# Kernel optimization log

Measured on AMD Instinct MI355X. Metric: run time of the kernel, lower is better.

The kernel has to match this reference:

```python
import jax, jax.numpy as jnp
import numpy as np

# Dimensions (see shape_source)
N, M, C = 64, 300, 768          # batch, tokens (=max_frames), token dim
LAMB, G, K = 2, 8, 64           # expansion, groups, clusters
GS = LAMB * C // G              # group_size = 192
DESC = K * GS                   # 12288 NeXtVLAD descriptor dim
NB, NCLS = 512, 701             # bottleneck, classes


def setup_inputs() -> dict:
    key = jax.random.key(0)
    ks = jax.random.split(key, 8)
    w = lambda i, shape: jax.random.normal(ks[i], shape, jnp.float32) * 0.02
    return {
        "features": jax.random.normal(ks[0], (N, M + 1, C), jnp.float32),
        # NeXtVLAD_block params
        "fc0_w": w(1, (LAMB * C, C)), "fc0_b": jnp.zeros((LAMB * C,), jnp.float32),
        "fcgk_w": w(2, (G * K, LAMB * C)), "fcgk_b": jnp.zeros((G * K,), jnp.float32),
        "fcg_w": w(3, (G, LAMB * C)), "fcg_b": jnp.zeros((G,), jnp.float32),
        "bn0_g": jnp.ones((M,), jnp.float32), "bn0_b": jnp.zeros((M,), jnp.float32),
        "cw2": jax.random.uniform(ks[4], (1, GS, K), jnp.float32),
        "bn1_g": jnp.ones((1,), jnp.float32), "bn1_b": jnp.zeros((1,), jnp.float32),
        # ClassBlock params (Linear -> BN -> Linear classifier)
        "cls_fc_w": w(5, (NB, DESC)), "cls_fc_b": jnp.zeros((NB,), jnp.float32),
        "cls_bn_g": jnp.ones((NB,), jnp.float32), "cls_bn_b": jnp.zeros((NB,), jnp.float32),
        "cls_w": w(6, (NCLS, NB)), "cls_b": jnp.zeros((NCLS,), jnp.float32),
    }


def reference(features, fc0_w, fc0_b, fcgk_w, fcgk_b, fcg_w, fcg_b,
              bn0_g, bn0_b, cw2, bn1_g, bn1_b,
              cls_fc_w, cls_fc_b, cls_bn_g, cls_bn_b, cls_w, cls_b):
    # Drop CLS token -> local descriptors (N, M, C). (transpose+vector2image
    # in the torch code is a pure rearrangement back to (N, M, C) tokens.)
    x = features[:, 1:]
    # 1) expand D -> lamb*D
    x_dot = jnp.einsum('nmc,ec->nme', x, fc0_w) + fc0_b           # (N, M, lamb*C)
    # 2) group: (N, M*G, group_size)
    x_tilde = x_dot.reshape(-1, M * G, GS)
    # 3) soft assignment logits, BN over the frame axis (inference-mode BN:
    #    running stats 0/1 -> pure per-frame affine), softmax over clusters
    WgkX = jnp.einsum('nme,fe->nmf', x_dot, fcgk_w) + fcgk_b      # (N, M, G*K)
    WgkX = WgkX * bn0_g[None, :, None] + bn0_b[None, :, None]
    alpha_gk = jax.nn.softmax(WgkX.reshape(-1, M * G, K), axis=-1)
    # 4) sigmoid group attention
    alpha_g = jax.nn.sigmoid(jnp.einsum('nme,ge->nmg', x_dot, fcg_w) + fcg_b)
    alpha_g = alpha_g.reshape(-1, M * G, 1)
    activation = alpha_gk * alpha_g                                # (N, M*G, K)
    # 5) aggregate residuals: vlad = act^T x_tilde - a_sum * centers
    a = jnp.sum(activation, axis=1, keepdims=True) * cw2           # (N, GS, K)
    vlad = jnp.einsum('npk,npd->ndk', activation, x_tilde) - a     # (N, GS, K)
    # 6) L1-normalize over group_size dim (F.normalize(vlad, 1): p=1, dim=1)
    norm = jnp.maximum(jnp.sum(jnp.abs(vlad), axis=1, keepdims=True), 1e-12)
    vlad = (vlad / norm).reshape(-1, DESC)
    # bn1 = BatchNorm1d(1), inference mode -> scalar affine
    vlad = vlad * bn1_g[0] + bn1_b[0]
    # ClassBlock: Linear -> BN (inference affine) -> classifier Linear
    f = jnp.einsum('nd,bd->nb', vlad, cls_fc_w) + cls_fc_b         # (N, NB)
    f = f * cls_bn_g + cls_bn_b
    cls = jnp.einsum('nb,cb->nc', f, cls_w) + cls_b                # (N, NCLS)
    return (cls, f)
```

## Files before the change

### kernel.cpp

```cpp
#include <hip/hip_runtime.h>
#include <hip/hip_bf16.h>

#define NN 64
#define MM 300
#define CC 768
#define EE 1536
#define GG 8
#define KK 64
#define FF 512
#define GS 192
#define PP 2400
#define DESC 12288
#define NMROWS 19200
#define NB 512
#define NCLS 701

typedef _Float16 v8h __attribute__((ext_vector_type(8)));
typedef _Float16 v4h __attribute__((ext_vector_type(4)));
typedef float    v4f __attribute__((ext_vector_type(4)));

#define GLOAD_LDS16(g, s) \
    __builtin_amdgcn_global_load_lds( \
        (const __attribute__((address_space(1))) void*)(g), \
        (__attribute__((address_space(3))) void*)(s), 16, 0, 0)

__global__ __launch_bounds__(256)
void pack_x_k(const float* __restrict__ f, _Float16* __restrict__ o)
{
    int idx = blockIdx.x * 256 + threadIdx.x;
    int row = idx / 192;
    int c4  = (idx - row * 192) * 4;
    int n = row / 300, m = row - n * 300;
    float4 v = *(const float4*)(f + ((size_t)(n * 301 + m + 1)) * CC + c4);
    v4h h = { (_Float16)v.x, (_Float16)v.y, (_Float16)v.z, (_Float16)v.w };
    *(v4h*)(o + (size_t)row * CC + c4) = h;
}

__global__ __launch_bounds__(256)
void pack_w_k(const float* __restrict__ s, _Float16* __restrict__ o, int n4)
{
    int idx = blockIdx.x * 256 + threadIdx.x;
    if (idx >= n4) return;
    float4 v = *(const float4*)(s + (size_t)idx * 4);
    v4h h = { (_Float16)v.x, (_Float16)v.y, (_Float16)v.z, (_Float16)v.w };
    *(v4h*)(o + (size_t)idx * 4) = h;
}

template<bool OUTF16, bool BN0, bool SOFTGATE>
__global__ __launch_bounds__(256)
void hgemm_nt(const _Float16* __restrict__ A, const _Float16* __restrict__ B,
              const float* __restrict__ bias,
              const float* __restrict__ bn_g, const float* __restrict__ bn_b,
              const float* __restrict__ sig,
              void* __restrict__ Cout, int Ndim, int Kdim)
{
    __shared__ _Float16 As[128 * 32];
    __shared__ _Float16 Bs[128 * 32];

    const int tid  = threadIdx.x;
    const int wave = tid >> 6, lane = tid & 63;
    const int wr   = wave >> 1, wc = wave & 1;
    const int row0 = blockIdx.y * 128, col0 = blockIdx.x * 128;

    const int l0 = tid, l1 = 256 + tid;
    const _Float16* ga0 = A + (size_t)(row0 + (l0 >> 2)) * Kdim + (l0 & 3) * 8;
    const _Float16* ga1 = A + (size_t)(row0 + (l1 >> 2)) * Kdim + (l1 & 3) * 8;
    const _Float16* gb0 = B + (size_t)(col0 + (l0 >> 2)) * Kdim + (l0 & 3) * 8;
    const _Float16* gb1 = B + (size_t)(col0 + (l1 >> 2)) * Kdim + (l1 & 3) * 8;
    _Float16* sa0 = As + wave * 512;
    _Float16* sa1 = As + 2048 + wave * 512;
    _Float16* sb0 = Bs + wave * 512;
    _Float16* sb1 = Bs + 2048 + wave * 512;

    v4f acc[4][4];
    #pragma unroll
    for (int i = 0; i < 4; ++i)
        #pragma unroll
        for (int j = 0; j < 4; ++j)
            acc[i][j] = (v4f){0.f, 0.f, 0.f, 0.f};

    const int fm = lane & 15, fq = lane >> 4;
    const _Float16* arp = As + (wr * 64 + fm) * 32 + fq * 8;
    const _Float16* brp = Bs + (wc * 64 + fm) * 32 + fq * 8;

    for (int kt = 0; kt < Kdim; kt += 32) {
        GLOAD_LDS16(ga0 + kt, sa0);
        GLOAD_LDS16(ga1 + kt, sa1);
        GLOAD_LDS16(gb0 + kt, sb0);
        GLOAD_LDS16(gb1 + kt, sb1);
        __syncthreads();

        v8h af[4], bf[4];
        #pragma unroll
        for (int i = 0; i < 4; ++i) af[i] = *(const v8h*)(arp + i * 16 * 32);
        #pragma unroll
        for (int j = 0; j < 4; ++j) bf[j] = *(const v8h*)(brp + j * 16 * 32);
        #pragma unroll
        for (int i = 0; i < 4; ++i)
            #pragma unroll
            for (int j = 0; j < 4; ++j)
                acc[i][j] = __builtin_amdgcn_mfma_f32_16x16x32_f16(
                    af[i], bf[j], acc[i][j], 0, 0, 0);
        __syncthreads();
    }

    float bj[4];
    #pragma unroll
    for (int j = 0; j < 4; ++j) bj[j] = bias[col0 + wc * 64 + j * 16 + fm];

    if (SOFTGATE) {
        const int gidx = (col0 >> 6) + wc;
        #pragma unroll
        for (int i = 0; i < 4; ++i) {
            #pragma unroll
            for (int r = 0; r < 4; ++r) {
                int grow = row0 + wr * 64 + i * 16 + fq * 4 + r;
                int n = grow / 300, mm = grow - n * 300;
                float g = bn_g[mm], bb = bn_b[mm];
                float v[4];
                #pragma unroll
                for (int j = 0; j < 4; ++j)
                    v[j] = (acc[i][j][r] + bj[j]) * g + bb;
                float mx = fmaxf(fmaxf(v[0], v[1]), fmaxf(v[2], v[3]));
                #pragma unroll
                for (int w = 1; w < 16; w <<= 1) mx = fmaxf(mx, __shfl_xor(mx, w));
                float e[4], s = 0.f;
                #pragma unroll
                for (int j = 0; j < 4; ++j) { e[j] = __expf(v[j] - mx); s += e[j]; }
                #pragma unroll
                for (int w = 1; w < 16; w <<= 1) s += __shfl_xor(s, w);
                float gate = sig[(size_t)grow * GG + gidx];
                float inv = gate / s;
                float* cp = (float*)Cout + (size_t)grow * Ndim + col0 + wc * 64;
                #pragma unroll
                for (int j = 0; j < 4; ++j) cp[j * 16 + fm] = e[j] * inv;
            }
        }
        return;
    }

    #pragma unroll
    for (int i = 0; i < 4; ++i) {
        #pragma unroll
        for (int r = 0; r < 4; ++r) {
            int grow = row0 + wr * 64 + i * 16 + fq * 4 + r;
            float g = 1.f, bb = 0.f;
            if (BN0) { int m = grow % 300; g = bn_g[m]; bb = bn_b[m]; }
            #pragma unroll
            for (int j = 0; j < 4; ++j) {
                int gcol = col0 + wc * 64 + j * 16 + fm;
                float v = acc[i][j][r] + bj[j];
                if (BN0) v = v * g + bb;
                if (OUTF16)
                    ((_Float16*)Cout)[(size_t)grow * Ndim + gcol] = (_Float16)v;
                else
                    ((float*)Cout)[(size_t)grow * Ndim + gcol] = v;
            }
        }
    }
}

__global__ __launch_bounds__(256)
void alpha_sig_k(const _Float16* __restrict__ xdot, const float* __restrict__ fcg_w,
                 const float* __restrict__ fcg_b, float* __restrict__ sig)
{
    __shared__ float W[GG * EE];
    for (int i = threadIdx.x; i < GG * EE; i += 256) W[i] = fcg_w[i];
    __syncthreads();

    const int wave = threadIdx.x >> 6;
    const int lane = threadIdx.x & 63;

    for (int rr = 0; rr < 4; ++rr) {
        int row = blockIdx.x * 16 + wave * 4 + rr;
        const _Float16* xr = xdot + (size_t)row * EE;
        float acc[GG] = {};
        for (int c = lane; c < EE; c += 64) {
            float xv = (float)xr[c];
            #pragma unroll
            for (int g = 0; g < GG; ++g) acc[g] = fmaf(xv, W[g * EE + c], acc[g]);
        }
        float myval = 0.f;
        #pragma unroll
        for (int g = 0; g < GG; ++g) {
            float s = acc[g];
            #pragma unroll
            for (int o = 32; o; o >>= 1) s += __shfl_xor(s, o);
            if (lane == g) myval = s + fcg_b[g];
        }
        if (lane < GG) {
            sig[(size_t)row * GG + lane] = 1.f / (1.f + __expf(-myval));
        }
    }
}

__global__ __launch_bounds__(256)
void asum_k(const float* __restrict__ act, float* __restrict__ a)
{
    int n = blockIdx.x;
    int k = threadIdx.x & 63, q = threadIdx.x >> 6;
    const float* base = act + (size_t)n * PP * 64;
    float s = 0.f;
    for (int p = q * 600; p < (q + 1) * 600; ++p) s += base[(size_t)p * 64 + k];
    __shared__ float part[4][64];
    part[q][k] = s;
    __syncthreads();
    if (threadIdx.x < 64)
        a[n * 64 + threadIdx.x] = part[0][threadIdx.x] + part[1][threadIdx.x]
                                + part[2][threadIdx.x] + part[3][threadIdx.x];
}

__global__ __launch_bounds__(256)
void vlad_ps_k(const float* __restrict__ act, const _Float16* __restrict__ xdot,
               float* __restrict__ part)
{
    const int dt = blockIdx.x, n = blockIdx.y, ps = blockIdx.z;
    const int d0 = dt * 64;
    const int p0 = ps * 300, pend = p0 + 300;
    __shared__ float As[16][64];
    __shared__ float Xs[16][64];
    const int tid = threadIdx.x;
    const int tx = tid & 15, ty = tid >> 4;
    const int kb = tx * 4, db = ty * 4;
    const float* actn = act + (size_t)n * PP * 64;
    const _Float16* xn = xdot + (size_t)n * MM * EE;
    float acc[4][4] = {};

    const int lpp = tid >> 4, lk4 = (tid & 15) << 2;
    for (int pc = p0; pc < pend; pc += 16) {
        int p = pc + lpp;
        float4 av = make_float4(0.f, 0.f, 0.f, 0.f);
        float x0 = 0.f, x1 = 0.f, x2 = 0.f, x3 = 0.f;
        if (p < pend) {
            av = *(const float4*)(actn + (size_t)p * 64 + lk4);
            v4h xv = *(const v4h*)(xn + (size_t)(p >> 3) * EE + (p & 7) * GS + d0 + lk4);
            x0 = (float)xv[0]; x1 = (float)xv[1]; x2 = (float)xv[2]; x3 = (float)xv[3];
        }
        *(float4*)&As[lpp][lk4] = av;
        Xs[lpp][lk4 + 0] = x0; Xs[lpp][lk4 + 1] = x1;
        Xs[lpp][lk4 + 2] = x2; Xs[lpp][lk4 + 3] = x3;
        __syncthreads();
        #pragma unroll
        for (int q = 0; q < 16; ++q) {
            float4 a4 = *(const float4*)&As[q][kb];
            float4 x4 = *(const float4*)&Xs[q][db];
            float aa[4] = {a4.x, a4.y, a4.z, a4.w};
            float xx[4] = {x4.x, x4.y, x4.z, x4.w};
            #pragma unroll
            for (int i = 0; i < 4; ++i)
                #pragma unroll
                for (int j = 0; j < 4; ++j)
                    acc[i][j] = fmaf(xx[i], aa[j], acc[i][j]);
        }
        __syncthreads();
    }

    float* pp = part + ((size_t)ps * NN + n) * DESC;
    #pragma unroll
    for (int i = 0; i < 4; ++i) {
        int dd = d0 + db + i;
        float4 o = {acc[i][0], acc[i][1], acc[i][2], acc[i][3]};
        *(float4*)(pp + (size_t)dd * 64 + kb) = o;
    }
}

__global__ __launch_bounds__(256)
void vlad_reduce_k(const float* __restrict__ part, const float* __restrict__ a,
                   const float* __restrict__ cw2, float* __restrict__ vlad)
{
    int idx = blockIdx.x * 256 + threadIdx.x;
    float s = 0.f;
    #pragma unroll
    for (int ps = 0; ps < 8; ++ps) s += part[(size_t)ps * (NN * DESC) + idx];
    int k = idx & 63;
    int d = (idx >> 6) % GS;
    int n = idx / DESC;
    vlad[idx] = s - a[n * 64 + k] * cw2[d * 64 + k];
}

__global__ __launch_bounds__(256)
void norm_k(float* __restrict__ vlad, const float* __restrict__ bn1g,
            const float* __restrict__ bn1b)
{
    int n = blockIdx.x;
    float* v = vlad + (size_t)n * DESC;
    int k = threadIdx.x & 63, q = threadIdx.x >> 6;
    float s = 0.f;
    for (int d = q * 48; d < q * 48 + 48; ++d) s += fabsf(v[d * 64 + k]);
    __shared__ float part[4][64];
    __shared__ float inv[64];
    part[q][k] = s;
    __syncthreads();
    if (threadIdx.x < 64) {
        float t = part[0][threadIdx.x] + part[1][threadIdx.x]
                + part[2][threadIdx.x] + part[3][threadIdx.x];
        inv[threadIdx.x] = 1.f / fmaxf(t, 1e-12f);
    }
    __syncthreads();
    float g = bn1g[0], b = bn1b[0];
    for (int idx = threadIdx.x; idx < DESC; idx += 256) {
        v[idx] = v[idx] * inv[idx & 63] * g + b;
    }
}

__global__ __launch_bounds__(256)
void fsplit_k(const float* __restrict__ vlad, const float* __restrict__ W,
              float* __restrict__ part)
{
    const int bcol0 = (blockIdx.x & 7) * 64;
    const int ks = blockIdx.x >> 3;
    const int kc0 = ks * 256;
    __shared__ float Vs[32][68];
    __shared__ float Ws[32][68];
    const int tid = threadIdx.x, tx = tid & 15, ty = tid >> 4;
    float acc[4][4] = {};

    for (int kc = kc0; kc < kc0 + 256; kc += 32) {
        #pragma unroll
        for (int it = 0; it < 2; ++it) {
            int sl = tid + it * 256;
            int rr = sl >> 3, k4 = (sl & 7) << 2;
            float4 v = *(const float4*)(vlad + (size_t)rr * DESC + kc + k4);
            Vs[k4+0][rr] = v.x; Vs[k4+1][rr] = v.y; Vs[k4+2][rr] = v.z; Vs[k4+3][rr] = v.w;
            float4 w = *(const float4*)(W + (size_t)(bcol0 + rr) * DESC + kc + k4);
            Ws[k4+0][rr] = w.x; Ws[k4+1][rr] = w.y; Ws[k4+2][rr] = w.z; Ws[k4+3][rr] = w.w;
        }
        __syncthreads();
        #pragma unroll
        for (int q = 0; q < 32; ++q) {
            float4 wv = *(const float4*)&Ws[q][tx*4];
            float4 vv = *(const float4*)&Vs[q][ty*4];
            float wa[4] = {wv.x, wv.y, wv.z, wv.w};
            float va[4] = {vv.x, vv.y, vv.z, vv.w};
            #pragma unroll
            for (int i = 0; i < 4; ++i)
                #pragma unroll
                for (int j = 0; j < 4; ++j)
                    acc[i][j] = fmaf(va[i], wa[j], acc[i][j]);
        }
        __syncthreads();
    }
    float* p = part + (size_t)ks * (NN * NB);
    #pragma unroll
    for (int i = 0; i < 4; ++i) {
        int n = ty * 4 + i;
        float4 o = {acc[i][0], acc[i][1], acc[i][2], acc[i][3]};
        *(float4*)(p + (size_t)n * NB + bcol0 + tx*4) = o;
    }
}

__global__ __launch_bounds__(256)
void freduce_k(const float* __restrict__ part, const float* __restrict__ bias,
               const float* __restrict__ bng, const float* __restrict__ bnb,
               float* __restrict__ f)
{
    int idx = blockIdx.x * 256 + threadIdx.x;
    float s = 0.f;
    for (int ks = 0; ks < 48; ++ks) s += part[(size_t)ks * (NN * NB) + idx];
    int b = idx & (NB - 1);
    f[idx] = (s + bias[b]) * bng[b] + bnb[b];
}

__global__ __launch_bounds__(256)
void cls_k(const float* __restrict__ f, const float* __restrict__ W,
           const float* __restrict__ bias, float* __restrict__ out)
{
    const int c0 = blockIdx.x * 64;
    __shared__ float Fs[32][68];
    __shared__ float Ws[32][68];
    const int tid = threadIdx.x, tx = tid & 15, ty = tid >> 4;
    float acc[4][4] = {};

    for (int kc = 0; kc < NB; kc += 32) {
        #pragma unroll
        for (int it = 0; it < 2; ++it) {
            int sl = tid + it * 256;
            int rr = sl >> 3, k4 = (sl & 7) << 2;
            float4 v = *(const float4*)(f + (size_t)rr * NB + kc + k4);
            Fs[k4+0][rr] = v.x; Fs[k4+1][rr] = v.y; Fs[k4+2][rr] = v.z; Fs[k4+3][rr] = v.w;
            int c = c0 + rr;
            float4 w = (c < NCLS) ? *(const float4*)(W + (size_t)c * NB + kc + k4)
                                  : make_float4(0.f, 0.f, 0.f, 0.f);
            Ws[k4+0][rr] = w.x; Ws[k4+1][rr] = w.y; Ws[k4+2][rr] = w.z; Ws[k4+3][rr] = w.w;
        }
        __syncthreads();
        #pragma unroll
        for (int q = 0; q < 32; ++q) {
            float4 wv = *(const float4*)&Ws[q][tx*4];
            float4 fv = *(const float4*)&Fs[q][ty*4];
            float wa[4] = {wv.x, wv.y, wv.z, wv.w};
            float fa[4] = {fv.x, fv.y, fv.z, fv.w};
            #pragma unroll
            for (int i = 0; i < 4; ++i)
                #pragma unroll
                for (int j = 0; j < 4; ++j)
                    acc[i][j] = fmaf(fa[i], wa[j], acc[i][j]);
        }
        __syncthreads();
    }
    #pragma unroll
    for (int i = 0; i < 4; ++i) {
        int n = ty * 4 + i;
        #pragma unroll
        for (int j = 0; j < 4; ++j) {
            int c = c0 + tx * 4 + j;
            if (c < NCLS) out[(size_t)n * NCLS + c] = acc[i][j] + bias[c];
        }
    }
}

extern "C" void kernel_launch(void* const* d_in, const int* in_sizes, int n_in,
                              void* d_out, int out_size, void* d_ws, size_t ws_size,
                              hipStream_t stream)
{
    const float* features = (const float*)d_in[0];
    const float* fc0_w    = (const float*)d_in[1];
    const float* fc0_b    = (const float*)d_in[2];
    const float* fcgk_w   = (const float*)d_in[3];
    const float* fcgk_b   = (const float*)d_in[4];
    const float* fcg_w    = (const float*)d_in[5];
    const float* fcg_b    = (const float*)d_in[6];
    const float* bn0_g    = (const float*)d_in[7];
    const float* bn0_b    = (const float*)d_in[8];
    const float* cw2      = (const float*)d_in[9];
    const float* bn1_g    = (const float*)d_in[10];
    const float* bn1_b    = (const float*)d_in[11];
    const float* cls_fc_w = (const float*)d_in[12];
    const float* cls_fc_b = (const float*)d_in[13];
    const float* cls_bn_g = (const float*)d_in[14];
    const float* cls_bn_b = (const float*)d_in[15];
    const float* cls_w    = (const float*)d_in[16];
    const float* cls_b    = (const float*)d_in[17];

    char* ws = (char*)d_ws;
    _Float16* xf16   = (_Float16*)(ws + 0);
    _Float16* w1f16  = (_Float16*)(ws + 29491200);
    _Float16* w2f16  = (_Float16*)(ws + 31850496);
    _Float16* xdot16 = (_Float16*)(ws + 33423360);
    float*    act    = (float*)   (ws + 92405760);
    float*    sigma  = (float*)   (ws + 131727360);
    float*    asum   = (float*)   (ws + 132341760);
    float*    vlad   = (float*)   (ws + 132358144);
    float*    vpart  = (float*)   (ws + 135503872);
    float*    fpart  = (float*)   (ws + 160669696);

    float* cls_out = (float*)d_out;
    float* f_out   = cls_out + NN * NCLS;

    dim3 blk(256);

    pack_x_k<<<14400, blk, 0, stream>>>(features, xf16);
    pack_w_k<<<1152, blk, 0, stream>>>(fc0_w, w1f16, EE * CC / 4);
    pack_w_k<<<768, blk, 0, stream>>>(fcgk_w, w2f16, FF * EE / 4);

    hgemm_nt<true, false, false><<<dim3(12, 150), blk, 0, stream>>>(
        xf16, w1f16, fc0_b, nullptr, nullptr, nullptr, xdot16, EE, CC);

    alpha_sig_k<<<1200, blk, 0, stream>>>(xdot16, fcg_w, fcg_b, sigma);

    hgemm_nt<false, true, true><<<dim3(4, 150), blk, 0, stream>>>(
        xdot16, w2f16, fcgk_b, bn0_g, bn0_b, sigma, act, FF, EE);

    asum_k<<<64, blk, 0, stream>>>(act, asum);

    vlad_ps_k<<<dim3(3, 64, 8), blk, 0, stream>>>(act, xdot16, vpart);
    vlad_reduce_k<<<3072, blk, 0, stream>>>(vpart, asum, cw2, vlad);

    norm_k<<<64, blk, 0, stream>>>(vlad, bn1_g, bn1_b);

    fsplit_k<<<384, blk, 0, stream>>>(vlad, cls_fc_w, fpart);
    freduce_k<<<128, blk, 0, stream>>>(fpart, cls_fc_b, cls_bn_g, cls_bn_b, f_out);

    cls_k<<<11, blk, 0, stream>>>(f_out, cls_w, cls_b, cls_out);
}
```

Measured before the change: 519.8 us.

## Fold fc0 into assignment and gate weights, swizzle LDS, store activations in fp16

```diff
diff --git a/kernel.cpp b/kernel.cpp
--- a/kernel.cpp
+++ b/kernel.cpp
@@ -46,7 +46,70 @@
     *(v4h*)(o + (size_t)idx * 4) = h;
 }
 
-template<bool OUTF16, bool BN0, bool SOFTGATE>
+__global__ __launch_bounds__(256)
+void transpose_w1_k(const float* __restrict__ w1, _Float16* __restrict__ o)
+{
+    __shared__ float T[64][65];
+    const int c0 = blockIdx.x * 64, e0 = blockIdx.y * 64;
+    const int tc = threadIdx.x & 63, te = threadIdx.x >> 6;
+    #pragma unroll
+    for (int r = 0; r < 16; ++r) {
+        int el = te * 16 + r;
+        T[el][tc] = w1[(size_t)(e0 + el) * CC + c0 + tc];
+    }
+    __syncthreads();
+    #pragma unroll
+    for (int r = 0; r < 16; ++r) {
+        int cl = te * 16 + r;
+        o[(size_t)(c0 + cl) * EE + e0 + tc] = (_Float16)T[tc][cl];
+    }
+}
+
+__global__ __launch_bounds__(256)
+void biasc_k(const float* __restrict__ w2, const float* __restrict__ b2,
+             const float* __restrict__ wg, const float* __restrict__ bg,
+             const float* __restrict__ b0, float* __restrict__ biasc)
+{
+    int f = blockIdx.x;
+    const float* row = (f < FF) ? (w2 + (size_t)f * EE) : (wg + (size_t)(f - FF) * EE);
+    float s = 0.f;
+    for (int e = threadIdx.x; e < EE; e += 256) s += row[e] * b0[e];
+    __shared__ float red[256];
+    red[threadIdx.x] = s;
+    __syncthreads();
+    for (int o = 128; o; o >>= 1) {
+        if (threadIdx.x < o) red[threadIdx.x] += red[threadIdx.x + o];
+        __syncthreads();
+    }
+    if (threadIdx.x == 0)
+        biasc[f] = red[0] + ((f < FF) ? b2[f] : bg[f - FF]);
+}
+
+__global__ __launch_bounds__(256)
+void wgc_k(const float* __restrict__ wg, const float* __restrict__ w1,
+           float* __restrict__ wgc)
+{
+    const int c = blockIdx.x * 64 + (threadIdx.x & 63);
+    const int q = threadIdx.x >> 6;
+    float acc[GG] = {};
+    for (int e = q * 384; e < q * 384 + 384; ++e) {
+        float w1v = w1[(size_t)e * CC + c];
+        #pragma unroll
+        for (int g = 0; g < GG; ++g) acc[g] = fmaf(wg[g * EE + e], w1v, acc[g]);
+    }
+    __shared__ float red[4][GG][64];
+    #pragma unroll
+    for (int g = 0; g < GG; ++g) red[q][g][threadIdx.x & 63] = acc[g];
+    __syncthreads();
+    if (threadIdx.x < 64) {
+        #pragma unroll
+        for (int g = 0; g < GG; ++g)
+            wgc[g * CC + c] = red[0][g][threadIdx.x] + red[1][g][threadIdx.x]
+                            + red[2][g][threadIdx.x] + red[3][g][threadIdx.x];
+    }
+}
+
+template<bool OUTF16, bool BN0, bool SOFTGATE, bool BIAS>
 __global__ __launch_bounds__(256)
 void hgemm_nt(const _Float16* __restrict__ A, const _Float16* __restrict__ B,
               const float* __restrict__ bias,
@@ -62,11 +125,12 @@
     const int wr   = wave >> 1, wc = wave & 1;
     const int row0 = blockIdx.y * 128, col0 = blockIdx.x * 128;
 
-    const int l0 = tid, l1 = 256 + tid;
-    const _Float16* ga0 = A + (size_t)(row0 + (l0 >> 2)) * Kdim + (l0 & 3) * 8;
-    const _Float16* ga1 = A + (size_t)(row0 + (l1 >> 2)) * Kdim + (l1 & 3) * 8;
-    const _Float16* gb0 = B + (size_t)(col0 + (l0 >> 2)) * Kdim + (l0 & 3) * 8;
-    const _Float16* gb1 = B + (size_t)(col0 + (l1 >> 2)) * Kdim + (l1 & 3) * 8;
+    const int r0 = tid >> 2, cs = tid & 3;
+    const int cc = cs ^ ((r0 >> 1) & 3);
+    const _Float16* ga0 = A + (size_t)(row0 + r0) * Kdim + cc * 8;
+    const _Float16* ga1 = A + (size_t)(row0 + r0 + 64) * Kdim + cc * 8;
+    const _Float16* gb0 = B + (size_t)(col0 + r0) * Kdim + cc * 8;
+    const _Float16* gb1 = B + (size_t)(col0 + r0 + 64) * Kdim + cc * 8;
     _Float16* sa0 = As + wave * 512;
     _Float16* sa1 = As + 2048 + wave * 512;
     _Float16* sb0 = Bs + wave * 512;
@@ -80,8 +144,9 @@
             acc[i][j] = (v4f){0.f, 0.f, 0.f, 0.f};
 
     const int fm = lane & 15, fq = lane >> 4;
-    const _Float16* arp = As + (wr * 64 + fm) * 32 + fq * 8;
-    const _Float16* brp = Bs + (wc * 64 + fm) * 32 + fq * 8;
+    const int sw = (fm >> 1) & 3;
+    const _Float16* arp = As + (wr * 64 + fm) * 32 + (fq ^ sw) * 8;
+    const _Float16* brp = Bs + (wc * 64 + fm) * 32 + (fq ^ sw) * 8;
 
     for (int kt = 0; kt < Kdim; kt += 32) {
         GLOAD_LDS16(ga0 + kt, sa0);
@@ -106,7 +171,8 @@
 
     float bj[4];
     #pragma unroll
-    for (int j = 0; j < 4; ++j) bj[j] = bias[col0 + wc * 64 + j * 16 + fm];
+    for (int j = 0; j < 4; ++j)
+        bj[j] = BIAS ? bias[col0 + wc * 64 + j * 16 + fm] : 0.f;
 
     if (SOFTGATE) {
         const int gidx = (col0 >> 6) + wc;
@@ -131,9 +197,15 @@
                 for (int w = 1; w < 16; w <<= 1) s += __shfl_xor(s, w);
                 float gate = sig[(size_t)grow * GG + gidx];
                 float inv = gate / s;
-                float* cp = (float*)Cout + (size_t)grow * Ndim + col0 + wc * 64;
-                #pragma unroll
-                for (int j = 0; j < 4; ++j) cp[j * 16 + fm] = e[j] * inv;
+                if (OUTF16) {
+                    _Float16* cp = (_Float16*)Cout + (size_t)grow * Ndim + col0 + wc * 64;
+                    #pragma unroll
+                    for (int j = 0; j < 4; ++j) cp[j * 16 + fm] = (_Float16)(e[j] * inv);
+                } else {
+                    float* cp = (float*)Cout + (size_t)grow * Ndim + col0 + wc * 64;
+                    #pragma unroll
+                    for (int j = 0; j < 4; ++j) cp[j * 16 + fm] = e[j] * inv;
+                }
             }
         }
         return;
@@ -161,11 +233,11 @@
 }
 
 __global__ __launch_bounds__(256)
-void alpha_sig_k(const _Float16* __restrict__ xdot, const float* __restrict__ fcg_w,
-                 const float* __restrict__ fcg_b, float* __restrict__ sig)
-{
-    __shared__ float W[GG * EE];
-    for (int i = threadIdx.x; i < GG * EE; i += 256) W[i] = fcg_w[i];
+void alpha_sig_k(const _Float16* __restrict__ x, const float* __restrict__ wgc,
+                 const float* __restrict__ bgc, float* __restrict__ sig)
+{
+    __shared__ float W[GG * CC];
+    for (int i = threadIdx.x; i < GG * CC; i += 256) W[i] = wgc[i];
     __syncthreads();
 
     const int wave = threadIdx.x >> 6;
@@ -173,12 +245,12 @@
 
     for (int rr = 0; rr < 4; ++rr) {
         int row = blockIdx.x * 16 + wave * 4 + rr;
-        const _Float16* xr = xdot + (size_t)row * EE;
+        const _Float16* xr = x + (size_t)row * CC;
         float acc[GG] = {};
-        for (int c = lane; c < EE; c += 64) {
+        for (int c = lane; c < CC; c += 64) {
             float xv = (float)xr[c];
             #pragma unroll
-            for (int g = 0; g < GG; ++g) acc[g] = fmaf(xv, W[g * EE + c], acc[g]);
+            for (int g = 0; g < GG; ++g) acc[g] = fmaf(xv, W[g * CC + c], acc[g]);
         }
         float myval = 0.f;
         #pragma unroll
@@ -186,7 +258,7 @@
             float s = acc[g];
             #pragma unroll
             for (int o = 32; o; o >>= 1) s += __shfl_xor(s, o);
-            if (lane == g) myval = s + fcg_b[g];
+            if (lane == g) myval = s + bgc[g];
         }
         if (lane < GG) {
             sig[(size_t)row * GG + lane] = 1.f / (1.f + __expf(-myval));
@@ -195,23 +267,24 @@
 }
 
 __global__ __launch_bounds__(256)
-void asum_k(const float* __restrict__ act, float* __restrict__ a)
-{
-    int n = blockIdx.x;
-    int k = threadIdx.x & 63, q = threadIdx.x >> 6;
-    const float* base = act + (size_t)n * PP * 64;
+void asum_ps_k(const _Float16* __restrict__ act, float* __restrict__ apart)
+{
+    const int ps = blockIdx.x, n = blockIdx.y;
+    const int k = threadIdx.x & 63, q = threadIdx.x >> 6;
+    const _Float16* base = act + ((size_t)n * PP + ps * 300 + q * 75) * 64 + k;
     float s = 0.f;
-    for (int p = q * 600; p < (q + 1) * 600; ++p) s += base[(size_t)p * 64 + k];
+    for (int p = 0; p < 75; ++p) s += (float)base[(size_t)p * 64];
     __shared__ float part[4][64];
     part[q][k] = s;
     __syncthreads();
     if (threadIdx.x < 64)
-        a[n * 64 + threadIdx.x] = part[0][threadIdx.x] + part[1][threadIdx.x]
-                                + part[2][threadIdx.x] + part[3][threadIdx.x];
-}
-
-__global__ __launch_bounds__(256)
-void vlad_ps_k(const float* __restrict__ act, const _Float16* __restrict__ xdot,
+        apart[((size_t)ps * NN + n) * 64 + threadIdx.x] =
+            part[0][threadIdx.x] + part[1][threadIdx.x]
+          + part[2][threadIdx.x] + part[3][threadIdx.x];
+}
+
+__global__ __launch_bounds__(256)
+void vlad_ps_k(const _Float16* __restrict__ act, const _Float16* __restrict__ xdot,
                float* __restrict__ part)
 {
     const int dt = blockIdx.x, n = blockIdx.y, ps = blockIdx.z;
@@ -222,21 +295,23 @@
     const int tid = threadIdx.x;
     const int tx = tid & 15, ty = tid >> 4;
     const int kb = tx * 4, db = ty * 4;
-    const float* actn = act + (size_t)n * PP * 64;
-    const _Float16* xn = xdot + (size_t)n * MM * EE;
+    const _Float16* actn = act + (size_t)n * PP * 64;
+    const _Float16* xn   = xdot + (size_t)n * MM * EE;
     float acc[4][4] = {};
 
     const int lpp = tid >> 4, lk4 = (tid & 15) << 2;
     for (int pc = p0; pc < pend; pc += 16) {
         int p = pc + lpp;
-        float4 av = make_float4(0.f, 0.f, 0.f, 0.f);
+        float a0 = 0.f, a1 = 0.f, a2 = 0.f, a3 = 0.f;
         float x0 = 0.f, x1 = 0.f, x2 = 0.f, x3 = 0.f;
         if (p < pend) {
-            av = *(const float4*)(actn + (size_t)p * 64 + lk4);
+            v4h avh = *(const v4h*)(actn + (size_t)p * 64 + lk4);
+            a0 = (float)avh[0]; a1 = (float)avh[1]; a2 = (float)avh[2]; a3 = (float)avh[3];
             v4h xv = *(const v4h*)(xn + (size_t)(p >> 3) * EE + (p & 7) * GS + d0 + lk4);
             x0 = (float)xv[0]; x1 = (float)xv[1]; x2 = (float)xv[2]; x3 = (float)xv[3];
         }
-        *(float4*)&As[lpp][lk4] = av;
+        As[lpp][lk4 + 0] = a0; As[lpp][lk4 + 1] = a1;
+        As[lpp][lk4 + 2] = a2; As[lpp][lk4 + 3] = a3;
         Xs[lpp][lk4 + 0] = x0; Xs[lpp][lk4 + 1] = x1;
         Xs[lpp][lk4 + 2] = x2; Xs[lpp][lk4 + 3] = x3;
         __syncthreads();
@@ -265,7 +340,7 @@
 }
 
 __global__ __launch_bounds__(256)
-void vlad_reduce_k(const float* __restrict__ part, const float* __restrict__ a,
+void vlad_reduce_k(const float* __restrict__ part, const float* __restrict__ apart,
                    const float* __restrict__ cw2, float* __restrict__ vlad)
 {
     int idx = blockIdx.x * 256 + threadIdx.x;
@@ -275,7 +350,10 @@
     int k = idx & 63;
     int d = (idx >> 6) % GS;
     int n = idx / DESC;
-    vlad[idx] = s - a[n * 64 + k] * cw2[d * 64 + k];
+    float a = 0.f;
+    #pragma unroll
+    for (int ps = 0; ps < 8; ++ps) a += apart[((size_t)ps * NN + n) * 64 + k];
+    vlad[idx] = s - a * cw2[d * 64 + k];
 }
 
 __global__ __launch_bounds__(256)
@@ -436,13 +514,17 @@
     _Float16* xf16   = (_Float16*)(ws + 0);
     _Float16* w1f16  = (_Float16*)(ws + 29491200);
     _Float16* w2f16  = (_Float16*)(ws + 31850496);
-    _Float16* xdot16 = (_Float16*)(ws + 33423360);
-    float*    act    = (float*)   (ws + 92405760);
-    float*    sigma  = (float*)   (ws + 131727360);
-    float*    asum   = (float*)   (ws + 132341760);
-    float*    vlad   = (float*)   (ws + 132358144);
-    float*    vpart  = (float*)   (ws + 135503872);
-    float*    fpart  = (float*)   (ws + 160669696);
+    _Float16* w1t16  = (_Float16*)(ws + 33423360);
+    _Float16* w2cf16 = (_Float16*)(ws + 35782656);
+    float*    biasc  = (float*)   (ws + 36569088);
+    float*    wgc    = (float*)   (ws + 36573184);
+    _Float16* xdot16 = (_Float16*)(ws + 36597760);
+    _Float16* act16  = (_Float16*)(ws + 95580160);
+    float*    sigma  = (float*)   (ws + 115240960);
+    float*    apart  = (float*)   (ws + 115855360);
+    float*    vpart  = (float*)   (ws + 115986432);
+    float*    vlad   = (float*)   (ws + 141152256);
+    float*    fpart  = (float*)   (ws + 144297984);
 
     float* cls_out = (float*)d_out;
     float* f_out   = cls_out + NN * NCLS;
@@ -452,19 +534,24 @@
     pack_x_k<<<14400, blk, 0, stream>>>(features, xf16);
     pack_w_k<<<1152, blk, 0, stream>>>(fc0_w, w1f16, EE * CC / 4);
     pack_w_k<<<768, blk, 0, stream>>>(fcgk_w, w2f16, FF * EE / 4);
-
-    hgemm_nt<true, false, false><<<dim3(12, 150), blk, 0, stream>>>(
+    transpose_w1_k<<<dim3(12, 24), blk, 0, stream>>>(fc0_w, w1t16);
+    biasc_k<<<520, blk, 0, stream>>>(fcgk_w, fcgk_b, fcg_w, fcg_b, fc0_b, biasc);
+    wgc_k<<<12, blk, 0, stream>>>(fcg_w, fc0_w, wgc);
+    hgemm_nt<true, false, false, false><<<dim3(6, 4), blk, 0, stream>>>(
+        w2f16, w1t16, nullptr, nullptr, nullptr, nullptr, w2cf16, CC, EE);
+
+    hgemm_nt<true, false, false, true><<<dim3(12, 150), blk, 0, stream>>>(
         xf16, w1f16, fc0_b, nullptr, nullptr, nullptr, xdot16, EE, CC);
 
-    alpha_sig_k<<<1200, blk, 0, stream>>>(xdot16, fcg_w, fcg_b, sigma);
-
-    hgemm_nt<false, true, true><<<dim3(4, 150), blk, 0, stream>>>(
-        xdot16, w2f16, fcgk_b, bn0_g, bn0_b, sigma, act, FF, EE);
-
-    asum_k<<<64, blk, 0, stream>>>(act, asum);
-
-    vlad_ps_k<<<dim3(3, 64, 8), blk, 0, stream>>>(act, xdot16, vpart);
-    vlad_reduce_k<<<3072, blk, 0, stream>>>(vpart, asum, cw2, vlad);
+    alpha_sig_k<<<1200, blk, 0, stream>>>(xf16, wgc, biasc + FF, sigma);
+
+    hgemm_nt<true, true, true, true><<<dim3(4, 150), blk, 0, stream>>>(
+        xf16, w2cf16, biasc, bn0_g, bn0_b, sigma, act16, FF, CC);
+
+    asum_ps_k<<<dim3(8, 64), blk, 0, stream>>>(act16, apart);
+
+    vlad_ps_k<<<dim3(3, 64, 8), blk, 0, stream>>>(act16, xdot16, vpart);
+    vlad_reduce_k<<<3072, blk, 0, stream>>>(vpart, apart, cw2, vlad);
 
     norm_k<<<64, blk, 0, stream>>>(vlad, bn1_g, bn1_b);
 
```

Result: no change. 510.7 us (-1.8%).
